# Kernel optimization log

Measured on AMD Instinct MI355X. Metric: run time of the kernel, lower is better.

The kernel has to match this reference:

```python
import jax, jax.numpy as jnp
import numpy as np

D_MODEL = 2048
EXP_RATE = 4
DEPTH = 1
EPS = 1e-5

def setup_inputs() -> dict:
    key = jax.random.key(0)
    k1, k2 = jax.random.split(key, 2)
    B, T, D, E = 4, 4096, D_MODEL, EXP_RATE
    x = jax.random.normal(k1, (B, T, D), dtype=jnp.float32)
    residual = jax.random.normal(k2, (B, T, D), dtype=jnp.float32)
    # static_alpha = cat([alpha0, eye(E)], dim=1) -> [E, E+1]
    alpha0 = np.zeros((E, 1), dtype=np.float32)
    alpha0[DEPTH % E, 0] = 1.0
    static_alpha = jnp.asarray(np.concatenate([alpha0, np.eye(E, dtype=np.float32)], axis=1))
    static_beta = jnp.ones((E,), dtype=jnp.float32)
    dynamic_alpha_fn = jnp.zeros((D, E + 1), dtype=jnp.float32)
    dynamic_alpha_scale = jnp.ones((1,), dtype=jnp.float32) * 0.01
    dynamic_beta_fn = jnp.zeros((D,), dtype=jnp.float32)
    dynamic_beta_scale = jnp.ones((1,), dtype=jnp.float32) * 0.01
    rms_weight = jnp.ones((D,), dtype=jnp.float32)
    return {
        "x": x, "residual": residual, "rms_weight": rms_weight,
        "static_alpha": static_alpha, "static_beta": static_beta,
        "dynamic_alpha_fn": dynamic_alpha_fn, "dynamic_alpha_scale": dynamic_alpha_scale,
        "dynamic_beta_fn": dynamic_beta_fn, "dynamic_beta_scale": dynamic_beta_scale,
    }

def reference(x, residual, rms_weight, static_alpha, static_beta,
              dynamic_alpha_fn, dynamic_alpha_scale, dynamic_beta_fn, dynamic_beta_scale):
    # RMSNorm (elementwise affine)
    norm_x = x * jax.lax.rsqrt(jnp.mean(x * x, axis=-1, keepdims=True) + EPS) * rms_weight
    # Dynamic params
    dyn_alpha = jnp.tanh(norm_x @ dynamic_alpha_fn) * dynamic_alpha_scale  # [B,T,E+1]
    dyn_beta = jnp.tanh(norm_x @ dynamic_beta_fn) * dynamic_beta_scale[0]  # [B,T]
    alpha = static_alpha[None, None] + dyn_alpha[:, :, None, :]  # [B,T,E,E+1]
    beta = static_beta[None, None] + dyn_beta[:, :, None]        # [B,T,E]
    # Width connection: einsum('btij,btjd->btid', alpha^T, x_expanded) with
    # x_expanded[b,t,j,:] == x[b,t,:] for all j  =>  mix_h[b,t,i,:] = (sum_j alpha[b,t,j,i]) * x[b,t,:]
    coeff = alpha.sum(axis=2)  # [B,T,E+1]
    # Depth connection: sum_e beta_e * residual + sum_{i>=1} mix_h_i  (dropout = identity at eval)
    out = residual * beta.sum(axis=-1, keepdims=True) + x * coeff[..., 1:].sum(axis=-1, keepdims=True)
    return out
```

## Files before the change

### kernel.cpp

```cpp
#include <hip/hip_runtime.h>


#define D_MODEL 2048
#define E_RATE 4
#define HC_EPS 1e-5f
#define NT 256
#define EPT 8

extern "C" __global__ void __launch_bounds__(NT)
hc_kernel(const float* __restrict__ x,
          const float* __restrict__ resid,
          const float* __restrict__ w,
          const float* __restrict__ sA,
          const float* __restrict__ sB,
          const float* __restrict__ fnA,
          const float* __restrict__ aScale,
          const float* __restrict__ fnB,
          const float* __restrict__ bScale,
          float* __restrict__ out)
{
    const int tid = threadIdx.x;
    const size_t rowBase = (size_t)blockIdx.x * D_MODEL;

    const float4* xr = (const float4*)(x + rowBase);
    float4 x0 = xr[2 * tid], x1 = xr[2 * tid + 1];
    float4 w0 = ((const float4*)w)[2 * tid];
    float4 w1 = ((const float4*)w)[2 * tid + 1];
    float4 b0 = ((const float4*)fnB)[2 * tid];
    float4 b1 = ((const float4*)fnB)[2 * tid + 1];

    float xf[EPT]  = {x0.x, x0.y, x0.z, x0.w, x1.x, x1.y, x1.z, x1.w};
    float wf[EPT]  = {w0.x, w0.y, w0.z, w0.w, w1.x, w1.y, w1.z, w1.w};
    float fbf[EPT] = {b0.x, b0.y, b0.z, b0.w, b1.x, b1.y, b1.z, b1.w};

    float xwp[EPT];
#pragma unroll
    for (int d = 0; d < EPT; d++) xwp[d] = xf[d] * wf[d];

    float vals[7];
#pragma unroll
    for (int j = 0; j < 7; j++) vals[j] = 0.0f;

#pragma unroll
    for (int d = 0; d < EPT; d++) {
        vals[6] += xf[d] * xf[d];
        vals[5] += xwp[d] * fbf[d];
    }

    const float4* fa4 = (const float4*)fnA;
#pragma unroll
    for (int j = 0; j < 10; j++) {
        float4 t4 = fa4[(size_t)tid * 10 + j];
        float fv[4] = {t4.x, t4.y, t4.z, t4.w};
#pragma unroll
        for (int q = 0; q < 4; q++) {
            const int e = j * 4 + q;
            const int d = e / 5;
            const int i = e % 5;
            vals[i] += xwp[d] * fv[q];
        }
    }

#pragma unroll
    for (int j = 0; j < 7; j++) {
        float v = vals[j];
        for (int off = 32; off > 0; off >>= 1) v += __shfl_xor(v, off, 64);
        vals[j] = v;
    }

    __shared__ float red[NT / 64][7];
    __shared__ float bc[2];
    const int wave = tid >> 6, lane = tid & 63;
    if (lane == 0) {
#pragma unroll
        for (int j = 0; j < 7; j++) red[wave][j] = vals[j];
    }
    __syncthreads();

    if (tid == 0) {
        float tot[7];
#pragma unroll
        for (int j = 0; j < 7; j++)
            tot[j] = red[0][j] + red[1][j] + red[2][j] + red[3][j];

        const float inv = rsqrtf(tot[6] * (1.0f / D_MODEL) + HC_EPS);
        const float asc = aScale[0];
        const float bsc = bScale[0];

        const float dynb = tanhf(tot[5] * inv) * bsc;
        float dyna_sum = 0.0f;
#pragma unroll
        for (int i = 1; i <= E_RATE; i++) dyna_sum += tanhf(tot[i] * inv) * asc;

        float SB = 0.0f;
#pragma unroll
        for (int e = 0; e < E_RATE; e++) SB += sB[e];
        float SA = 0.0f;
#pragma unroll
        for (int i = 1; i <= E_RATE; i++)
#pragma unroll
            for (int j = 0; j < E_RATE; j++) SA += sA[j * (E_RATE + 1) + i];

        bc[0] = SB + (float)E_RATE * dynb;
        bc[1] = SA + (float)E_RATE * dyna_sum;
    }
    __syncthreads();

    const float cR = bc[0], cX = bc[1];

    const float4* rr = (const float4*)(resid + rowBase);
    float4 r0 = rr[2 * tid], r1 = rr[2 * tid + 1];

    float4 o0, o1;
    o0.x = r0.x * cR + xf[0] * cX;
    o0.y = r0.y * cR + xf[1] * cX;
    o0.z = r0.z * cR + xf[2] * cX;
    o0.w = r0.w * cR + xf[3] * cX;
    o1.x = r1.x * cR + xf[4] * cX;
    o1.y = r1.y * cR + xf[5] * cX;
    o1.z = r1.z * cR + xf[6] * cX;
    o1.w = r1.w * cR + xf[7] * cX;

    float4* orow = (float4*)(out + rowBase);
    orow[2 * tid]     = o0;
    orow[2 * tid + 1] = o1;
}

extern "C" void kernel_launch(void* const* d_in, const int* in_sizes, int n_in,
                              void* d_out, int out_size, void* d_ws, size_t ws_size,
                              hipStream_t stream) {
    const float* x      = (const float*)d_in[0];
    const float* resid  = (const float*)d_in[1];
    const float* w      = (const float*)d_in[2];
    const float* sA     = (const float*)d_in[3];
    const float* sB     = (const float*)d_in[4];
    const float* fnA    = (const float*)d_in[5];
    const float* aScale = (const float*)d_in[6];
    const float* fnB    = (const float*)d_in[7];
    const float* bScale = (const float*)d_in[8];
    float* out          = (float*)d_out;

    const int n_tokens = in_sizes[0] / D_MODEL;

    hc_kernel<<<n_tokens, NT, 0, stream>>>(x, resid, w, sA, sB, fnA, aScale,
                                           fnB, bScale, out);
}
```

Before: 390.8 us.

## Use persistent wave-per-token kernel with prefolded weights in LDS and x prefetch

The kernel becomes persistent: a fixed grid of blocks, where each wave handles one token at a time and strides across tokens. The rms weight is prefolded into the dynamic-alpha and dynamic-beta projection vectors once per block and kept in shared memory. The next token's x row is prefetched into registers while the current token is processed. Per-token reductions now use only wave shuffles, removing block-level syncs and the single-thread epilogue, and tanh is replaced by a fast exp-based form. This costs a large register footprint and 40KB of LDS per block, which limits occupancy.

```diff
diff --git a/kernel.cpp b/kernel.cpp
--- a/kernel.cpp
+++ b/kernel.cpp
@@ -5,9 +5,20 @@
 #define E_RATE 4
 #define HC_EPS 1e-5f
 #define NT 256
-#define EPT 8
+#define GRID 2048
 
-extern "C" __global__ void __launch_bounds__(NT)
+__device__ __forceinline__ float tanh_fast(float v) {
+    float e = __expf(2.0f * v);
+    return 1.0f - 2.0f / (e + 1.0f);
+}
+
+__device__ __forceinline__ float wave_sum(float v) {
+#pragma unroll
+    for (int off = 32; off > 0; off >>= 1) v += __shfl_xor(v, off, 64);
+    return v;
+}
+
+extern "C" __global__ void __launch_bounds__(NT, 3)
 hc_kernel(const float* __restrict__ x,
           const float* __restrict__ resid,
           const float* __restrict__ w,
@@ -17,113 +28,114 @@
           const float* __restrict__ aScale,
           const float* __restrict__ fnB,
           const float* __restrict__ bScale,
-          float* __restrict__ out)
+          float* __restrict__ out,
+          int n_tokens)
 {
-    const int tid = threadIdx.x;
-    const size_t rowBase = (size_t)blockIdx.x * D_MODEL;
+    __shared__ __align__(16) float P[5][D_MODEL];
 
-    const float4* xr = (const float4*)(x + rowBase);
-    float4 x0 = xr[2 * tid], x1 = xr[2 * tid + 1];
-    float4 w0 = ((const float4*)w)[2 * tid];
-    float4 w1 = ((const float4*)w)[2 * tid + 1];
-    float4 b0 = ((const float4*)fnB)[2 * tid];
-    float4 b1 = ((const float4*)fnB)[2 * tid + 1];
+    const int tid  = threadIdx.x;
+    const int lane = tid & 63;
+    const int wave = tid >> 6;
 
-    float xf[EPT]  = {x0.x, x0.y, x0.z, x0.w, x1.x, x1.y, x1.z, x1.w};
-    float wf[EPT]  = {w0.x, w0.y, w0.z, w0.w, w1.x, w1.y, w1.z, w1.w};
-    float fbf[EPT] = {b0.x, b0.y, b0.z, b0.w, b1.x, b1.y, b1.z, b1.w};
-
-    float xwp[EPT];
+    {
+        const int d8 = tid * 8;
+        float4 w0 = ((const float4*)w)[2 * tid];
+        float4 w1 = ((const float4*)w)[2 * tid + 1];
+        float4 b0 = ((const float4*)fnB)[2 * tid];
+        float4 b1 = ((const float4*)fnB)[2 * tid + 1];
+        float w8[8] = {w0.x, w0.y, w0.z, w0.w, w1.x, w1.y, w1.z, w1.w};
+        float f8[8] = {b0.x, b0.y, b0.z, b0.w, b1.x, b1.y, b1.z, b1.w};
+        float fa[40];
+        float4* fap = (float4*)fa;
+        const float4* fnA4 = (const float4*)fnA;
 #pragma unroll
-    for (int d = 0; d < EPT; d++) xwp[d] = xf[d] * wf[d];
-
-    float vals[7];
+        for (int j = 0; j < 10; j++) fap[j] = fnA4[tid * 10 + j];
 #pragma unroll
-    for (int j = 0; j < 7; j++) vals[j] = 0.0f;
-
+        for (int k = 0; k < 8; k++) {
 #pragma unroll
-    for (int d = 0; d < EPT; d++) {
-        vals[6] += xf[d] * xf[d];
-        vals[5] += xwp[d] * fbf[d];
-    }
-
-    const float4* fa4 = (const float4*)fnA;
-#pragma unroll
-    for (int j = 0; j < 10; j++) {
-        float4 t4 = fa4[(size_t)tid * 10 + j];
-        float fv[4] = {t4.x, t4.y, t4.z, t4.w};
-#pragma unroll
-        for (int q = 0; q < 4; q++) {
-            const int e = j * 4 + q;
-            const int d = e / 5;
-            const int i = e % 5;
-            vals[i] += xwp[d] * fv[q];
+            for (int i = 0; i < 4; i++) P[i][d8 + k] = w8[k] * fa[k * 5 + (i + 1)];
+            P[4][d8 + k] = w8[k] * f8[k];
         }
     }
 
+    const float SB = sB[0] + sB[1] + sB[2] + sB[3];
+    float SA = 0.0f;
 #pragma unroll
-    for (int j = 0; j < 7; j++) {
-        float v = vals[j];
-        for (int off = 32; off > 0; off >>= 1) v += __shfl_xor(v, off, 64);
-        vals[j] = v;
+    for (int j = 0; j < 4; j++)
+#pragma unroll
+        for (int i = 1; i <= 4; i++) SA += sA[j * 5 + i];
+    const float asc = aScale[0];
+    const float bsc = bScale[0];
+
+    __syncthreads();
+
+    const int gw0 = blockIdx.x * (NT / 64) + wave;
+    const int nGW = GRID * (NT / 64);
+
+    float4 xc[8];
+    int tk = gw0;
+    if (tk < n_tokens) {
+        const float4* xr = (const float4*)(x + (size_t)tk * D_MODEL);
+#pragma unroll
+        for (int c = 0; c < 8; c++) xc[c] = xr[c * 64 + lane];
     }
 
-    __shared__ float red[NT / 64][7];
-    __shared__ float bc[2];
-    const int wave = tid >> 6, lane = tid & 63;
-    if (lane == 0) {
+    for (; tk < n_tokens; tk += nGW) {
+        const int nxt = tk + nGW;
+
+        float4 rc[8];
+        const float4* rr = (const float4*)(resid + (size_t)tk * D_MODEL);
 #pragma unroll
-        for (int j = 0; j < 7; j++) red[wave][j] = vals[j];
+        for (int c = 0; c < 8; c++) rc[c] = rr[c * 64 + lane];
+
+        float4 xn[8];
+        if (nxt < n_tokens) {
+            const float4* xr = (const float4*)(x + (size_t)nxt * D_MODEL);
+#pragma unroll
+            for (int c = 0; c < 8; c++) xn[c] = xr[c * 64 + lane];
+        }
+
+        float a0 = 0, a1 = 0, a2 = 0, a3 = 0, ab = 0, ssq = 0;
+#pragma unroll
+        for (int c = 0; c < 8; c++) {
+            const float4 xv = xc[c];
+            const int off = c * 256 + lane * 4;
+            const float4 p0 = *(const float4*)&P[0][off];
+            const float4 p1 = *(const float4*)&P[1][off];
+            const float4 p2 = *(const float4*)&P[2][off];
+            const float4 p3 = *(const float4*)&P[3][off];
+            const float4 pb = *(const float4*)&P[4][off];
+            ssq += xv.x * xv.x + xv.y * xv.y + xv.z * xv.z + xv.w * xv.w;
+            a0  += xv.x * p0.x + xv.y * p0.y + xv.z * p0.z + xv.w * p0.w;
+            a1  += xv.x * p1.x + xv.y * p1.y + xv.z * p1.z + xv.w * p1.w;
+            a2  += xv.x * p2.x + xv.y * p2.y + xv.z * p2.z + xv.w * p2.w;
+            a3  += xv.x * p3.x + xv.y * p3.y + xv.z * p3.z + xv.w * p3.w;
+            ab  += xv.x * pb.x + xv.y * pb.y + xv.z * pb.z + xv.w * pb.w;
+        }
+
+        a0 = wave_sum(a0); a1 = wave_sum(a1); a2 = wave_sum(a2);
+        a3 = wave_sum(a3); ab = wave_sum(ab); ssq = wave_sum(ssq);
+
+        const float inv = rsqrtf(ssq * (1.0f / D_MODEL) + HC_EPS);
+        const float dynA = tanh_fast(a0 * inv) + tanh_fast(a1 * inv) +
+                           tanh_fast(a2 * inv) + tanh_fast(a3 * inv);
+        const float cX = SA + (float)E_RATE * asc * dynA;
+        const float cR = SB + (float)E_RATE * bsc * tanh_fast(ab * inv);
+
+        float4* orow = (float4*)(out + (size_t)tk * D_MODEL);
+#pragma unroll
+        for (int c = 0; c < 8; c++) {
+            float4 o;
+            o.x = rc[c].x * cR + xc[c].x * cX;
+            o.y = rc[c].y * cR + xc[c].y * cX;
+            o.z = rc[c].z * cR + xc[c].z * cX;
+            o.w = rc[c].w * cR + xc[c].w * cX;
+            orow[c * 64 + lane] = o;
+        }
+
+#pragma unroll
+        for (int c = 0; c < 8; c++) xc[c] = xn[c];
     }
-    __syncthreads();
-
-    if (tid == 0) {
-        float tot[7];
-#pragma unroll
-        for (int j = 0; j < 7; j++)
-            tot[j] = red[0][j] + red[1][j] + red[2][j] + red[3][j];
-
-        const float inv = rsqrtf(tot[6] * (1.0f / D_MODEL) + HC_EPS);
-        const float asc = aScale[0];
-        const float bsc = bScale[0];
-
-        const float dynb = tanhf(tot[5] * inv) * bsc;
-        float dyna_sum = 0.0f;
-#pragma unroll
-        for (int i = 1; i <= E_RATE; i++) dyna_sum += tanhf(tot[i] * inv) * asc;
-
-        float SB = 0.0f;
-#pragma unroll
-        for (int e = 0; e < E_RATE; e++) SB += sB[e];
-        float SA = 0.0f;
-#pragma unroll
-        for (int i = 1; i <= E_RATE; i++)
-#pragma unroll
-            for (int j = 0; j < E_RATE; j++) SA += sA[j * (E_RATE + 1) + i];
-
-        bc[0] = SB + (float)E_RATE * dynb;
-        bc[1] = SA + (float)E_RATE * dyna_sum;
-    }
-    __syncthreads();
-
-    const float cR = bc[0], cX = bc[1];
-
-    const float4* rr = (const float4*)(resid + rowBase);
-    float4 r0 = rr[2 * tid], r1 = rr[2 * tid + 1];
-
-    float4 o0, o1;
-    o0.x = r0.x * cR + xf[0] * cX;
-    o0.y = r0.y * cR + xf[1] * cX;
-    o0.z = r0.z * cR + xf[2] * cX;
-    o0.w = r0.w * cR + xf[3] * cX;
-    o1.x = r1.x * cR + xf[4] * cX;
-    o1.y = r1.y * cR + xf[5] * cX;
-    o1.z = r1.z * cR + xf[6] * cX;
-    o1.w = r1.w * cR + xf[7] * cX;
-
-    float4* orow = (float4*)(out + rowBase);
-    orow[2 * tid]     = o0;
-    orow[2 * tid + 1] = o1;
 }
 
 extern "C" void kernel_launch(void* const* d_in, const int* in_sizes, int n_in,
@@ -142,6 +154,6 @@
 
     const int n_tokens = in_sizes[0] / D_MODEL;
 
-    hc_kernel<<<n_tokens, NT, 0, stream>>>(x, resid, w, sA, sB, fnA, aScale,
-                                           fnB, bScale, out);
+    hc_kernel<<<GRID, NT, 0, stream>>>(x, resid, w, sA, sB, fnA, aScale,
+                                       fnB, bScale, out, n_tokens);
 }
```

After: 493.7 us. +26.3%, slower.
